# Kernel optimization log

Hardware: AMD Instinct MI355X
Metric: run time of the kernel (lower is better)

Reference implementation:

```python
import jax, jax.numpy as jnp
import numpy as np

B, L, HID, D, H, HKV, EPS, THETA = 1, 2048, 2048, 128, 32, 4, 1e-6, 1000000.0
GROUPS = H // HKV  # 8


def setup_inputs() -> dict:
    key = jax.random.key(0)
    ks = jax.random.split(key, 6)
    x = jax.random.normal(ks[0], (B, L, HID), dtype=jnp.float32)
    wq = jax.random.normal(ks[1], (H * D, HID), dtype=jnp.float32) * 0.02
    wk = jax.random.normal(ks[2], (HKV * D, HID), dtype=jnp.float32) * 0.02
    wv = jax.random.normal(ks[3], (HKV * D, HID), dtype=jnp.float32) * 0.02
    wo = jax.random.normal(ks[4], (HID, H * D), dtype=jnp.float32) * 0.02
    q_norm_w = jnp.ones((D,), dtype=jnp.float32)
    k_norm_w = jnp.ones((D,), dtype=jnp.float32)
    # RoPE tables: inv_freq over half dims, emb = concat(freqs, freqs)
    inv_freq = 1.0 / (THETA ** (jnp.arange(0, D, 2, dtype=jnp.float32) / D))
    pos = jnp.arange(L, dtype=jnp.float32)
    freqs = pos[:, None] * inv_freq[None, :]        # [L, D/2]
    emb = jnp.concatenate([freqs, freqs], axis=-1)  # [L, D]
    cos = jnp.cos(emb)[None]                        # [1, L, D]
    sin = jnp.sin(emb)[None]
    return {"x": x, "wq": wq, "wk": wk, "wv": wv, "wo": wo,
            "q_norm_w": q_norm_w, "k_norm_w": k_norm_w, "cos": cos, "sin": sin}


def _rmsnorm(t, w):
    var = jnp.mean(t * t, axis=-1, keepdims=True)
    return t * jax.lax.rsqrt(var + EPS) * w


def _rotate_half(t):
    t1, t2 = jnp.split(t, 2, axis=-1)
    return jnp.concatenate([-t2, t1], axis=-1)


def reference(x, wq, wk, wv, wo, q_norm_w, k_norm_w, cos, sin):
    b, l, _ = x.shape
    # projections -> [B, heads, L, D]
    q = _rmsnorm((x @ wq.T).reshape(b, l, H, D), q_norm_w).swapaxes(1, 2)
    k = _rmsnorm((x @ wk.T).reshape(b, l, HKV, D), k_norm_w).swapaxes(1, 2)
    v = (x @ wv.T).reshape(b, l, HKV, D).swapaxes(1, 2)
    # RoPE (cos/sin broadcast over head dim)
    c, s = cos[:, None], sin[:, None]
    q = c * q + s * _rotate_half(q)
    k = c * k + s * _rotate_half(k)
    # GQA: repeat kv heads across groups
    k = jnp.repeat(k, GROUPS, axis=1)
    v = jnp.repeat(v, GROUPS, axis=1)
    # causal SDPA
    scores = jnp.einsum("bhqd,bhkd->bhqk", q, k) / np.sqrt(D).astype(np.float32)
    causal = jnp.tril(jnp.ones((l, l), dtype=bool))
    scores = jnp.where(causal, scores, jnp.finfo(scores.dtype).min)
    attn = jax.nn.softmax(scores, axis=-1)
    out = jnp.einsum("bhqk,bhkd->bhqd", attn, v)
    out = out.swapaxes(1, 2).reshape(b, l, H * D)
    return out @ wo.T
```

## Files before the change

### kernel.cpp

```cpp
#include <hip/hip_runtime.h>

typedef unsigned short u16;
typedef short bh8 __attribute__((ext_vector_type(8)));
typedef short bh4 __attribute__((ext_vector_type(4)));
typedef float f4 __attribute__((ext_vector_type(4)));
typedef u16 u16x4 __attribute__((ext_vector_type(4)));

__device__ __forceinline__ u16 f2bf(float f) {
  union { float f; unsigned u; } v; v.f = f;
  unsigned u = v.u;
  return (u16)((u + 0x7fffu + ((u >> 16) & 1u)) >> 16);
}
__device__ __forceinline__ float bf2f(u16 h) {
  union { unsigned u; float f; } v; v.u = ((unsigned)h) << 16;
  return v.f;
}
__device__ __forceinline__ float fast_exp2(float x) {
#if __has_builtin(__builtin_amdgcn_exp2f)
  return __builtin_amdgcn_exp2f(x);
#else
  float r; asm("v_exp_f32 %0, %1" : "=v"(r) : "v"(x)); return r;
#endif
}
__device__ __forceinline__ unsigned cvt_pk_bf16(float lo, float hi) {
  unsigned r;
  asm("v_cvt_pk_bf16_f32 %0, %1, %2" : "=v"(r) : "v"(lo), "v"(hi));
  return r;
}
__device__ __forceinline__ void gll16(const void* src, void* dst) {
  __builtin_amdgcn_global_load_lds((const __attribute__((address_space(1))) void*)src,
                                   (__attribute__((address_space(3))) void*)dst,
                                   16, 0, 0);
}

__global__ __launch_bounds__(256) void k_cvt_all(const float* __restrict__ x,
                                                 const float* __restrict__ wq,
                                                 const float* __restrict__ wk,
                                                 const float* __restrict__ wv,
                                                 const float* __restrict__ wo,
                                                 u16* __restrict__ dst) {
  const size_t n = 5767168;
  for (size_t idx = (size_t)blockIdx.x * 256 + threadIdx.x; idx < n; idx += 4096ull * 256) {
    const float* src; size_t off;
    if (idx < 1048576)       { src = x;  off = idx; }
    else if (idx < 3145728)  { src = wq; off = idx - 1048576; }
    else if (idx < 3407872)  { src = wk; off = idx - 3145728; }
    else if (idx < 3670016)  { src = wv; off = idx - 3407872; }
    else                     { src = wo; off = idx - 3670016; }
    f4 v = *(const f4*)(src + off * 4);
    u16x4 o;
    o.x = f2bf(v[0]); o.y = f2bf(v[1]); o.z = f2bf(v[2]); o.w = f2bf(v[3]);
    *(u16x4*)(dst + idx * 4) = o;
  }
}

template<int K, bool OUTF32, int NFR, bool FUSED>
__global__ __launch_bounds__(256) void k_gemm(const u16* __restrict__ A,
                                              const u16* __restrict__ B1,
                                              const u16* __restrict__ B2,
                                              void* __restrict__ C1,
                                              void* __restrict__ C2,
                                              u16* __restrict__ Cv,
                                              int N1, int N2, int NB1, int npx,
                                              int nbK) {
  constexpr int BN = NFR * 32;
  constexpr int nk = K / 32;
  constexpr int LBB = BN / 64;
  __shared__ u16 As[3][128 * 32];
  __shared__ u16 Bs[3][BN * 32];
  const int t = threadIdx.x;
  const int lane = t & 63;
  const int w = t >> 6, wm = w >> 1, wn = w & 1;
  const int g = lane >> 4, r16 = lane & 15;
  const int bb = blockIdx.x;
  const int gl = (bb & 7) * npx + (bb >> 3);
  const int bm = gl & 15;
  int bn = gl >> 4;

  const u16* B; void* C; int N; bool vpath = false;
  if (!FUSED || bn < NB1) { B = B1; C = C1; N = N1; }
  else { bn -= NB1; B = B2; C = C2; N = N2; vpath = (bn >= nbK); }
  B += (size_t)bn * BN * K;
  const u16* Ab = A + (size_t)bm * 128 * K;

  f4 acc[4][NFR] = {};

  auto STAGE = [&](int kk, int bi) {
    const int k0 = kk * 32;
#pragma unroll
    for (int i2 = 0; i2 < 2; ++i2) {
      const int s = t + 256 * i2;
      const int row = s >> 2, slot = s & 3;
      gll16(Ab + (size_t)row * K + k0 + ((slot ^ (row & 3)) * 8), As[bi] + s * 8);
    }
#pragma unroll
    for (int i2 = 0; i2 < LBB; ++i2) {
      const int s = t + 256 * i2;
      const int col = s >> 2, slot = s & 3;
      gll16(B + (size_t)col * K + k0 + ((slot ^ (col & 3)) * 8), Bs[bi] + s * 8);
    }
  };
  auto COMP = [&](int bi) {
    bh8 af[4], bfr[NFR];
    const int x4 = g ^ (r16 & 3);
#pragma unroll
    for (int m = 0; m < 4; ++m)
      af[m] = *(const bh8*)&As[bi][((wm * 64 + m * 16 + r16) * 4 + x4) * 8];
#pragma unroll
    for (int n = 0; n < NFR; ++n)
      bfr[n] = *(const bh8*)&Bs[bi][((wn * 16 * NFR + n * 16 + r16) * 4 + x4) * 8];
    __builtin_amdgcn_s_setprio(1);
#pragma unroll
    for (int m = 0; m < 4; ++m)
#pragma unroll
      for (int n = 0; n < NFR; ++n)
        acc[m][n] = __builtin_amdgcn_mfma_f32_16x16x32_bf16(af[m], bfr[n], acc[m][n], 0, 0, 0);
    __builtin_amdgcn_s_setprio(0);
  };

  STAGE(0, 0);
  STAGE(1, 1);

  int bi = 0;
  for (int k = 0; k < nk - 2; ++k) {
    int st = bi + 2; if (st >= 3) st -= 3;
    STAGE(k + 2, st);
    if constexpr (NFR == 4) asm volatile("s_waitcnt vmcnt(8)" ::: "memory");
    else                    asm volatile("s_waitcnt vmcnt(6)" ::: "memory");
    __builtin_amdgcn_s_barrier();
    __builtin_amdgcn_sched_barrier(0);
    COMP(bi);
    asm volatile("s_waitcnt lgkmcnt(0)" ::: "memory");
    __builtin_amdgcn_s_barrier();
    bi = (bi + 1 == 3) ? 0 : bi + 1;
  }
  if constexpr (NFR == 4) asm volatile("s_waitcnt vmcnt(4)" ::: "memory");
  else                    asm volatile("s_waitcnt vmcnt(3)" ::: "memory");
  __builtin_amdgcn_s_barrier();
  __builtin_amdgcn_sched_barrier(0);
  COMP(bi);
  asm volatile("s_waitcnt lgkmcnt(0)" ::: "memory");
  __builtin_amdgcn_s_barrier();
  bi = (bi + 1 == 3) ? 0 : bi + 1;
  asm volatile("s_waitcnt vmcnt(0)" ::: "memory");
  __builtin_amdgcn_s_barrier();
  __builtin_amdgcn_sched_barrier(0);
  COMP(bi);

  if constexpr (FUSED) {
    if (vpath) {
#pragma unroll
      for (int m = 0; m < 4; ++m) {
        const int lp = bm * 128 + wm * 64 + (m >> 1) * 32 + g * 8 + (m & 1) * 4;
#pragma unroll
        for (int n = 0; n < NFR; ++n) {
          const int col = bn * BN + wn * 16 * NFR + n * 16 + r16;
          union { u16x4 v; unsigned wrd[2]; } o;
          o.wrd[0] = cvt_pk_bf16(acc[m][n][0], acc[m][n][1]);
          o.wrd[1] = cvt_pk_bf16(acc[m][n][2], acc[m][n][3]);
          *(u16x4*)&Cv[(size_t)(col - 512) * 2048 + lp] = o.v;
        }
      }
      return;
    }
  }

#pragma unroll
  for (int m = 0; m < 4; ++m) {
    const int row0 = bm * 128 + wm * 64 + m * 16 + g * 4;
#pragma unroll
    for (int n = 0; n < NFR; ++n) {
      const int col = bn * BN + wn * 16 * NFR + n * 16 + r16;
#pragma unroll
      for (int r = 0; r < 4; ++r) {
        if constexpr (OUTF32)
          ((float*)C)[(size_t)(row0 + r) * N + col] = acc[m][n][r];
        else
          ((u16*)C)[(size_t)(row0 + r) * N + col] = f2bf(acc[m][n][r]);
      }
    }
  }
}

template<int K, int NFR>
__global__ __launch_bounds__(256) void k_gemm_sk(const u16* __restrict__ A,
                                                 const u16* __restrict__ Bw,
                                                 float* __restrict__ C0,
                                                 float* __restrict__ C1p,
                                                 int N, int npx) {
  constexpr int BN = NFR * 32;
  constexpr int KLEN = K / 2;
  constexpr int nk = KLEN / 32;
  constexpr int LBB = BN / 64;
  __shared__ u16 As[3][128 * 32];
  __shared__ u16 Bs[3][BN * 32];
  const int t = threadIdx.x;
  const int lane = t & 63;
  const int w = t >> 6, wm = w >> 1, wn = w & 1;
  const int g = lane >> 4, r16 = lane & 15;
  const int bb = blockIdx.x;
  int gl = (bb & 7) * npx + (bb >> 3);
  const int ks = gl >> 9; gl &= 511;
  const int bm = gl & 15;
  const int bn = gl >> 4;
  float* C = ks ? C1p : C0;
  const u16* B  = Bw + (size_t)bn * BN * K + ks * KLEN;
  const u16* Ab = A  + (size_t)bm * 128 * K + ks * KLEN;

  f4 acc[4][NFR] = {};

  auto STAGE = [&](int kk, int bi) {
    const int k0 = kk * 32;
#pragma unroll
    for (int i2 = 0; i2 < 2; ++i2) {
      const int s = t + 256 * i2;
      const int row = s >> 2, slot = s & 3;
      gll16(Ab + (size_t)row * K + k0 + ((slot ^ (row & 3)) * 8), As[bi] + s * 8);
    }
#pragma unroll
    for (int i2 = 0; i2 < LBB; ++i2) {
      const int s = t + 256 * i2;
      const int col = s >> 2, slot = s & 3;
      gll16(B + (size_t)col * K + k0 + ((slot ^ (col & 3)) * 8), Bs[bi] + s * 8);
    }
  };
  auto COMP = [&](int bi) {
    bh8 af[4], bfr[NFR];
    const int x4 = g ^ (r16 & 3);
#pragma unroll
    for (int m = 0; m < 4; ++m)
      af[m] = *(const bh8*)&As[bi][((wm * 64 + m * 16 + r16) * 4 + x4) * 8];
#pragma unroll
    for (int n = 0; n < NFR; ++n)
      bfr[n] = *(const bh8*)&Bs[bi][((wn * 16 * NFR + n * 16 + r16) * 4 + x4) * 8];
    __builtin_amdgcn_s_setprio(1);
#pragma unroll
    for (int m = 0; m < 4; ++m)
#pragma unroll
      for (int n = 0; n < NFR; ++n)
        acc[m][n] = __builtin_amdgcn_mfma_f32_16x16x32_bf16(af[m], bfr[n], acc[m][n], 0, 0, 0);
    __builtin_amdgcn_s_setprio(0);
  };

  STAGE(0, 0);
  STAGE(1, 1);

  int bi = 0;
  for (int k = 0; k < nk - 2; ++k) {
    int st = bi + 2; if (st >= 3) st -= 3;
    STAGE(k + 2, st);
    asm volatile("s_waitcnt vmcnt(6)" ::: "memory");
    __builtin_amdgcn_s_barrier();
    __builtin_amdgcn_sched_barrier(0);
    COMP(bi);
    asm volatile("s_waitcnt lgkmcnt(0)" ::: "memory");
    __builtin_amdgcn_s_barrier();
    bi = (bi + 1 == 3) ? 0 : bi + 1;
  }
  asm volatile("s_waitcnt vmcnt(3)" ::: "memory");
  __builtin_amdgcn_s_barrier();
  __builtin_amdgcn_sched_barrier(0);
  COMP(bi);
  asm volatile("s_waitcnt lgkmcnt(0)" ::: "memory");
  __builtin_amdgcn_s_barrier();
  bi = (bi + 1 == 3) ? 0 : bi + 1;
  asm volatile("s_waitcnt vmcnt(0)" ::: "memory");
  __builtin_amdgcn_s_barrier();
  __builtin_amdgcn_sched_barrier(0);
  COMP(bi);

#pragma unroll
  for (int m = 0; m < 4; ++m) {
    const int row0 = bm * 128 + wm * 64 + m * 16 + g * 4;
#pragma unroll
    for (int n = 0; n < NFR; ++n) {
      const int col = bn * BN + wn * 16 * NFR + n * 16 + r16;
#pragma unroll
      for (int r = 0; r < 4; ++r)
        C[(size_t)(row0 + r) * N + col] = acc[m][n][r];
    }
  }
}

__global__ __launch_bounds__(256) void k_reduce(float* __restrict__ out,
                                                const float* __restrict__ part) {
  const size_t i = (size_t)blockIdx.x * 256 + threadIdx.x;
  f4 a = *(const f4*)(out + i * 4);
  f4 b = *(const f4*)(part + i * 4);
  a += b;
  *(f4*)(out + i * 4) = a;
}

__global__ __launch_bounds__(256) void k_normrope(u16* __restrict__ qbuf,
                                                  u16* __restrict__ kvbuf,
                                                  const float* __restrict__ qw,
                                                  const float* __restrict__ kw,
                                                  const float* __restrict__ cosb,
                                                  const float* __restrict__ sinb) {
  const float CSC = 1.4426950408889634f * 0.088388347648318447f;
  const int t = threadIdx.x, lane = t & 63, w = t >> 6;
  const int rid = blockIdx.x * 4 + w;
  u16* base; const float* nw; int seq; float sc;
  if (rid < 2048 * 32) {
    seq = rid >> 5;
    base = qbuf + (size_t)seq * 4096 + (size_t)(rid & 31) * 128;
    nw = qw; sc = CSC;
  } else {
    const int r2 = rid - 2048 * 32;
    seq = r2 >> 2;
    base = kvbuf + (size_t)seq * 1024 + (size_t)(r2 & 3) * 128;
    nw = kw; sc = 1.0f;
  }
  float a = bf2f(base[lane]);
  float b = bf2f(base[lane + 64]);
  float ss = a * a + b * b;
#pragma unroll
  for (int off = 32; off >= 1; off >>= 1) ss += __shfl_xor(ss, off);
  const float rs = rsqrtf(ss * (1.0f / 128.0f) + 1e-6f);
  const float na = a * rs * nw[lane];
  const float nb = b * rs * nw[lane + 64];
  const float c1 = cosb[seq * 128 + lane],      s1 = sinb[seq * 128 + lane];
  const float c2 = cosb[seq * 128 + lane + 64], s2 = sinb[seq * 128 + lane + 64];
  base[lane]      = f2bf(sc * (c1 * na - s1 * nb));
  base[lane + 64] = f2bf(sc * (c2 * nb + s2 * na));
}

__global__ __launch_bounds__(512, 4) void k_attn(const u16* __restrict__ Q,
                                                 const u16* __restrict__ Kb,
                                                 const u16* __restrict__ Vt,
                                                 u16* __restrict__ O) {
  __shared__ u16 Ks[2][64 * 128];
  __shared__ u16 Vs[128 * 64];
  const int t = threadIdx.x, lane = t & 63, w = t >> 6;
  const int g = lane >> 4, r16 = lane & 15;
  const int b = blockIdx.x;
  const int i = b & 31;
  const int j = b >> 5;
  const int qt = (j < 8) ? (15 - j) : (j - 8);
  const int h = ((i >> 1) & 3) * 8 + ((i & 1) << 2) + (i >> 3);
  const int kvh = h >> 3;
  const int qw0 = qt * 128 + w * 16;
  const int qg  = qw0 + r16;

  bh8 qf[4];
#pragma unroll
  for (int kc = 0; kc < 4; ++kc)
    qf[kc] = *(const bh8*)(Q + (size_t)qg * 4096 + h * 128 + (kc * 4 + g) * 8);

  const int niter = 2 * qt + 2;

  f4 acc_o[8] = {};
  f4 acc_l = {};
  float mrun = -3.0e38f;

  bh8 ones;
#pragma unroll
  for (int z = 0; z < 8; ++z) ones[z] = (short)0x3F80;

#pragma unroll
  for (int i2 = 0; i2 < 2; ++i2) {
    const int s = t + 512 * i2, row = s >> 4, sl = s & 15;
    gll16(Kb + (size_t)row * 1024 + kvh * 128 + ((sl ^ (row & 15)) * 8), Ks[0] + s * 8);
  }
  __syncthreads();

  int cur = 0;
  for (int kt = 0; kt < niter; ++kt) {
#pragma unroll
    for (int i2 = 0; i2 < 2; ++i2) {
      const int s = t + 512 * i2, row = s >> 3, sl = s & 7;
      gll16(Vt + (size_t)(kvh * 128 + row) * 2048 + kt * 64 + ((sl ^ (row & 7)) * 8),
            Vs + s * 8);
    }
    if (kt + 1 < niter) {
      const int nt = kt + 1;
#pragma unroll
      for (int i2 = 0; i2 < 2; ++i2) {
        const int s = t + 512 * i2, row = s >> 4, sl = s & 15;
        gll16(Kb + (size_t)(nt * 64 + row) * 1024 + kvh * 128 + ((sl ^ (row & 15)) * 8),
              Ks[cur ^ 1] + s * 8);
      }
    }

    f4 st[4] = {};
    __builtin_amdgcn_s_setprio(1);
#pragma unroll
    for (int kf = 0; kf < 4; ++kf) {
      const int krow = kf * 16 + r16;
#pragma unroll
      for (int kc = 0; kc < 4; ++kc) {
        bh8 kfr = *(const bh8*)&Ks[cur][krow * 128 + (((kc * 4 + g) ^ (krow & 15)) * 8)];
        st[kf] = __builtin_amdgcn_mfma_f32_16x16x32_bf16(kfr, qf[kc], st[kf], 0, 0, 0);
      }
    }
    __builtin_amdgcn_s_setprio(0);

    if (kt >= 2 * qt) {
      const int kb = kt * 64 + g * 4;
#pragma unroll
      for (int kf = 0; kf < 4; ++kf)
#pragma unroll
        for (int r = 0; r < 4; ++r)
          if (kb + kf * 16 + r > qg) st[kf][r] = -3.0e38f;
    }

    f4 m4;
#pragma unroll
    for (int r = 0; r < 4; ++r)
      m4[r] = fmaxf(fmaxf(st[0][r], st[1][r]), fmaxf(st[2][r], st[3][r]));
    float tmax = fmaxf(fmaxf(m4[0], m4[1]), fmaxf(m4[2], m4[3]));
    tmax = fmaxf(tmax, __shfl_xor(tmax, 16));
    tmax = fmaxf(tmax, __shfl_xor(tmax, 32));

    if (!__all(tmax <= mrun + 8.0f)) {
      const float mnew = fmaxf(mrun, tmax);
      const float alpha = fast_exp2(mrun - mnew);
      mrun = mnew;
      acc_l *= alpha;
#pragma unroll
      for (int d = 0; d < 8; ++d) acc_o[d] *= alpha;
    }

    union { bh8 v[2]; unsigned wrd[8]; } pu;
#pragma unroll
    for (int j2 = 0; j2 < 8; ++j2) {
      const int i0 = 2 * j2, i1 = 2 * j2 + 1;
      float p0 = fast_exp2(st[i0 >> 2][i0 & 3] - mrun);
      float p1 = fast_exp2(st[i1 >> 2][i1 & 3] - mrun);
      pu.wrd[j2] = cvt_pk_bf16(p0, p1);
    }

    __syncthreads();

    __builtin_amdgcn_s_setprio(1);
#pragma unroll
    for (int c = 0; c < 2; ++c)
      acc_l = __builtin_amdgcn_mfma_f32_16x16x32_bf16(ones, pu.v[c], acc_l, 0, 0, 0);
#pragma unroll
    for (int dcol = 0; dcol < 8; ++dcol) {
      const int vrow = dcol * 16 + r16;
#pragma unroll
      for (int c = 0; c < 2; ++c) {
        const int slot = c * 4 + g;
        bh8 vfr = *(const bh8*)&Vs[vrow * 64 + ((slot ^ (vrow & 7)) * 8)];
        acc_o[dcol] = __builtin_amdgcn_mfma_f32_16x16x32_bf16(vfr, pu.v[c], acc_o[dcol], 0, 0, 0);
      }
    }
    __builtin_amdgcn_s_setprio(0);

    __syncthreads();
    cur ^= 1;
  }

  const float inv = 1.0f / acc_l[0];
#pragma unroll
  for (int dcol = 0; dcol < 8; ++dcol) {
    union { u16x4 v; unsigned wrd[2]; } o;
    o.wrd[0] = cvt_pk_bf16(acc_o[dcol][0] * inv, acc_o[dcol][1] * inv);
    o.wrd[1] = cvt_pk_bf16(acc_o[dcol][2] * inv, acc_o[dcol][3] * inv);
    *(u16x4*)&O[(size_t)qg * 4096 + h * 128 + dcol * 16 + g * 4] = o.v;
  }
}

extern "C" void kernel_launch(void* const* d_in, const int* in_sizes, int n_in,
                              void* d_out, int out_size, void* d_ws, size_t ws_size,
                              hipStream_t stream) {
  (void)in_sizes; (void)n_in; (void)out_size; (void)ws_size;
  const float* x    = (const float*)d_in[0];
  const float* wq   = (const float*)d_in[1];
  const float* wk   = (const float*)d_in[2];
  const float* wv   = (const float*)d_in[3];
  const float* wo   = (const float*)d_in[4];
  const float* qw   = (const float*)d_in[5];
  const float* kw   = (const float*)d_in[6];
  const float* cosb = (const float*)d_in[7];
  const float* sinb = (const float*)d_in[8];

  u16* xb   = (u16*)d_ws;
  u16* wqb  = xb  + (size_t)2048 * 2048;
  u16* wkvb = wqb + (size_t)4096 * 2048;
  u16* wob  = wkvb + (size_t)1024 * 2048;
  u16* qbuf = wob + (size_t)2048 * 4096;
  u16* kvb  = qbuf + (size_t)2048 * 4096;
  u16* vt   = kvb + (size_t)2048 * 1024;
  u16* aout = vt  + (size_t)512 * 2048;
  float* partial = (float*)wqb;

  k_cvt_all<<<dim3(4096), 256, 0, stream>>>(x, wq, wk, wv, wo, xb);

  k_gemm<2048, false, 4, true><<<dim3(640), 256, 0, stream>>>(
      xb, wqb, wkvb, qbuf, kvb, vt, 4096, 1024, 32, 80, 4);

  k_normrope<<<dim3((2048 * 36) / 4), 256, 0, stream>>>(qbuf, kvb, qw, kw, cosb, sinb);

  k_attn<<<dim3(512), 512, 0, stream>>>(qbuf, kvb, vt, aout);

  k_gemm_sk<4096, 2><<<dim3(1024), 256, 0, stream>>>(
      aout, wob, (float*)d_out, partial, 2048, 128);

  k_reduce<<<dim3(4096), 256, 0, stream>>>((float*)d_out, partial);
}
```

Baseline: 197.2 us.

## Fuse RMSNorm and RoPE into the QKV projection GEMM epilogue

Removes the separate norm+rope kernel by computing per-row sums of squares across the two wn warps via shared memory, normalizing, staging through LDS, and applying RoPE before writing Q/K. This saves a full read/write pass over Q and K plus a kernel launch. In exchange, the GEMM epilogue gains extra barriers, LDS traffic and global cos/sin loads, and only half the warps do the final stores with strided 2-byte writes.

```diff
diff --git a/kernel.cpp b/kernel.cpp
--- a/kernel.cpp
+++ b/kernel.cpp
@@ -61,13 +61,19 @@
                                               void* __restrict__ C1,
                                               void* __restrict__ C2,
                                               u16* __restrict__ Cv,
+                                              const float* __restrict__ qw,
+                                              const float* __restrict__ kw,
+                                              const float* __restrict__ cosb,
+                                              const float* __restrict__ sinb,
                                               int N1, int N2, int NB1, int npx,
                                               int nbK) {
   constexpr int BN = NFR * 32;
   constexpr int nk = K / 32;
   constexpr int LBB = BN / 64;
-  __shared__ u16 As[3][128 * 32];
-  __shared__ u16 Bs[3][BN * 32];
+  constexpr int ASZ = 3 * 128 * 32;
+  __shared__ u16 smem[ASZ + 3 * BN * 32];
+  u16* AsB = smem;
+  u16* BsB = smem + ASZ;
   const int t = threadIdx.x;
   const int lane = t & 63;
   const int w = t >> 6, wm = w >> 1, wn = w & 1;
@@ -76,6 +82,7 @@
   const int gl = (bb & 7) * npx + (bb >> 3);
   const int bm = gl & 15;
   int bn = gl >> 4;
+  const bool isQ = (!FUSED) || (bn < NB1);
 
   const u16* B; void* C; int N; bool vpath = false;
   if (!FUSED || bn < NB1) { B = B1; C = C1; N = N1; }
@@ -91,13 +98,13 @@
     for (int i2 = 0; i2 < 2; ++i2) {
       const int s = t + 256 * i2;
       const int row = s >> 2, slot = s & 3;
-      gll16(Ab + (size_t)row * K + k0 + ((slot ^ (row & 3)) * 8), As[bi] + s * 8);
+      gll16(Ab + (size_t)row * K + k0 + ((slot ^ (row & 3)) * 8), AsB + bi * 4096 + s * 8);
     }
 #pragma unroll
     for (int i2 = 0; i2 < LBB; ++i2) {
       const int s = t + 256 * i2;
       const int col = s >> 2, slot = s & 3;
-      gll16(B + (size_t)col * K + k0 + ((slot ^ (col & 3)) * 8), Bs[bi] + s * 8);
+      gll16(B + (size_t)col * K + k0 + ((slot ^ (col & 3)) * 8), BsB + bi * BN * 32 + s * 8);
     }
   };
   auto COMP = [&](int bi) {
@@ -105,10 +112,10 @@
     const int x4 = g ^ (r16 & 3);
 #pragma unroll
     for (int m = 0; m < 4; ++m)
-      af[m] = *(const bh8*)&As[bi][((wm * 64 + m * 16 + r16) * 4 + x4) * 8];
+      af[m] = *(const bh8*)&AsB[bi * 4096 + ((wm * 64 + m * 16 + r16) * 4 + x4) * 8];
 #pragma unroll
     for (int n = 0; n < NFR; ++n)
-      bfr[n] = *(const bh8*)&Bs[bi][((wn * 16 * NFR + n * 16 + r16) * 4 + x4) * 8];
+      bfr[n] = *(const bh8*)&BsB[bi * BN * 32 + ((wn * 16 * NFR + n * 16 + r16) * 4 + x4) * 8];
     __builtin_amdgcn_s_setprio(1);
 #pragma unroll
     for (int m = 0; m < 4; ++m)
@@ -163,6 +170,70 @@
       }
       return;
     }
+    float ssqp[4][4];
+#pragma unroll
+    for (int m = 0; m < 4; ++m)
+#pragma unroll
+      for (int r = 0; r < 4; ++r) {
+        float s = 0.0f;
+#pragma unroll
+        for (int n = 0; n < NFR; ++n) s += acc[m][n][r] * acc[m][n][r];
+#pragma unroll
+        for (int off = 8; off >= 1; off >>= 1) s += __shfl_xor(s, off);
+        ssqp[m][r] = s;
+      }
+    __builtin_amdgcn_s_barrier();
+    float* ssq = (float*)(smem + 16384);
+    if (r16 == 0) {
+#pragma unroll
+      for (int m = 0; m < 4; ++m)
+#pragma unroll
+        for (int r = 0; r < 4; ++r)
+          ssq[(wm * 64 + m * 16 + g * 4 + r) * 2 + wn] = ssqp[m][r];
+    }
+    asm volatile("s_waitcnt lgkmcnt(0)" ::: "memory");
+    __builtin_amdgcn_s_barrier();
+    u16* T = smem;
+    const float* nw = isQ ? qw : kw;
+    float nwv[NFR];
+#pragma unroll
+    for (int n = 0; n < NFR; ++n) nwv[n] = nw[wn * 64 + n * 16 + r16];
+#pragma unroll
+    for (int m = 0; m < 4; ++m)
+#pragma unroll
+      for (int r = 0; r < 4; ++r) {
+        const int row = wm * 64 + m * 16 + g * 4 + r;
+        const float rs = rsqrtf((ssq[row * 2] + ssq[row * 2 + 1]) * (1.0f / 128.0f) + 1e-6f);
+#pragma unroll
+        for (int n = 0; n < NFR; ++n)
+          T[row * 128 + wn * 64 + n * 16 + r16] = f2bf(acc[m][n][r] * rs * nwv[n]);
+      }
+    asm volatile("s_waitcnt lgkmcnt(0)" ::: "memory");
+    __builtin_amdgcn_s_barrier();
+    if (wn == 0) {
+      const float CSC = 1.4426950408889634f * 0.088388347648318447f;
+      const float sc = isQ ? CSC : 1.0f;
+      u16* Cq = (u16*)C;
+#pragma unroll
+      for (int m = 0; m < 4; ++m)
+#pragma unroll
+        for (int r = 0; r < 4; ++r) {
+          const int row = wm * 64 + m * 16 + g * 4 + r;
+          const int seq = bm * 128 + row;
+#pragma unroll
+          for (int n = 0; n < NFR; ++n) {
+            const int d = n * 16 + r16;
+            const float a  = bf2f(T[row * 128 + d]);
+            const float b2 = bf2f(T[row * 128 + d + 64]);
+            const float c1 = cosb[seq * 128 + d],      s1 = sinb[seq * 128 + d];
+            const float c2 = cosb[seq * 128 + d + 64], s2 = sinb[seq * 128 + d + 64];
+            const int colb = bn * BN + d;
+            Cq[(size_t)seq * N + colb]      = f2bf(sc * (c1 * a - s1 * b2));
+            Cq[(size_t)seq * N + colb + 64] = f2bf(sc * (c2 * b2 + s2 * a));
+          }
+        }
+    }
+    return;
   }
 
 #pragma unroll
@@ -291,40 +362,6 @@
   *(f4*)(out + i * 4) = a;
 }
 
-__global__ __launch_bounds__(256) void k_normrope(u16* __restrict__ qbuf,
-                                                  u16* __restrict__ kvbuf,
-                                                  const float* __restrict__ qw,
-                                                  const float* __restrict__ kw,
-                                                  const float* __restrict__ cosb,
-                                                  const float* __restrict__ sinb) {
-  const float CSC = 1.4426950408889634f * 0.088388347648318447f;
-  const int t = threadIdx.x, lane = t & 63, w = t >> 6;
-  const int rid = blockIdx.x * 4 + w;
-  u16* base; const float* nw; int seq; float sc;
-  if (rid < 2048 * 32) {
-    seq = rid >> 5;
-    base = qbuf + (size_t)seq * 4096 + (size_t)(rid & 31) * 128;
-    nw = qw; sc = CSC;
-  } else {
-    const int r2 = rid - 2048 * 32;
-    seq = r2 >> 2;
-    base = kvbuf + (size_t)seq * 1024 + (size_t)(r2 & 3) * 128;
-    nw = kw; sc = 1.0f;
-  }
-  float a = bf2f(base[lane]);
-  float b = bf2f(base[lane + 64]);
-  float ss = a * a + b * b;
-#pragma unroll
-  for (int off = 32; off >= 1; off >>= 1) ss += __shfl_xor(ss, off);
-  const float rs = rsqrtf(ss * (1.0f / 128.0f) + 1e-6f);
-  const float na = a * rs * nw[lane];
-  const float nb = b * rs * nw[lane + 64];
-  const float c1 = cosb[seq * 128 + lane],      s1 = sinb[seq * 128 + lane];
-  const float c2 = cosb[seq * 128 + lane + 64], s2 = sinb[seq * 128 + lane + 64];
-  base[lane]      = f2bf(sc * (c1 * na - s1 * nb));
-  base[lane + 64] = f2bf(sc * (c2 * nb + s2 * na));
-}
-
 __global__ __launch_bounds__(512, 4) void k_attn(const u16* __restrict__ Q,
                                                  const u16* __restrict__ Kb,
                                                  const u16* __restrict__ Vt,
@@ -489,9 +526,7 @@
   k_cvt_all<<<dim3(4096), 256, 0, stream>>>(x, wq, wk, wv, wo, xb);
 
   k_gemm<2048, false, 4, true><<<dim3(640), 256, 0, stream>>>(
-      xb, wqb, wkvb, qbuf, kvb, vt, 4096, 1024, 32, 80, 4);
-
-  k_normrope<<<dim3((2048 * 36) / 4), 256, 0, stream>>>(qbuf, kvb, qw, kw, cosb, sinb);
+      xb, wqb, wkvb, qbuf, kvb, vt, qw, kw, cosb, sinb, 4096, 1024, 32, 80, 4);
 
   k_attn<<<dim3(512), 512, 0, stream>>>(qbuf, kvb, vt, aout);
 
```

After: 215.1 us. 9.0% more time.
